# Optimization experiments

Hardware: AMD Instinct MI355X
Metric: run time of the kernel (lower is better)

Reference implementation:

```python
import jax, jax.numpy as jnp
import numpy as np

D_MODEL = 1024
NUM_HEAD = 16
HEAD_DIM = D_MODEL // NUM_HEAD  # 64


def setup_inputs() -> dict:
    key = jax.random.key(0)
    ks = jax.random.split(key, 9)
    B, S = 2, 2048
    s = 0.02
    return {
        "x": jax.random.normal(ks[0], (B, S, D_MODEL), dtype=jnp.float32),
        "Wq": jax.random.normal(ks[1], (D_MODEL, D_MODEL), dtype=jnp.float32) * s,
        "bq": jax.random.normal(ks[2], (D_MODEL,), dtype=jnp.float32) * s,
        "Wk": jax.random.normal(ks[3], (D_MODEL, D_MODEL), dtype=jnp.float32) * s,
        "bk": jax.random.normal(ks[4], (D_MODEL,), dtype=jnp.float32) * s,
        "Wv": jax.random.normal(ks[5], (D_MODEL, D_MODEL), dtype=jnp.float32) * s,
        "bv": jax.random.normal(ks[6], (D_MODEL,), dtype=jnp.float32) * s,
        "Wo": jax.random.normal(ks[7], (D_MODEL, D_MODEL), dtype=jnp.float32) * s,
        "bo": jax.random.normal(ks[8], (D_MODEL,), dtype=jnp.float32) * s,
    }


def _split_head(t):
    # [B,S,D] -> [B,H,S,hd]
    B, S, _ = t.shape
    return t.reshape(B, S, NUM_HEAD, HEAD_DIM).transpose(0, 2, 1, 3)


def reference(x, Wq, bq, Wk, bk, Wv, bv, Wo, bo):
    B, S, D = x.shape
    q = _split_head(x @ Wq.T + bq)  # [B,H,S,hd]
    k = _split_head(x @ Wk.T + bk)
    v = _split_head(x @ Wv.T + bv)
    scale = 1.0 / jnp.sqrt(jnp.asarray(HEAD_DIM, dtype=x.dtype))
    scores = jnp.einsum("bhqd,bhkd->bhqk", q, k) * scale  # [B,H,S,S]
    attn = jax.nn.softmax(scores, axis=-1)
    out = jnp.einsum("bhqk,bhkd->bhqd", attn, v)  # [B,H,S,hd]
    out = out.transpose(0, 2, 1, 3).reshape(B, S, D)
    return out @ Wo.T + bo
```

## Files before the change

### kernel.cpp

```cpp
#include <hip/hip_runtime.h>
#include <cstdint>


typedef unsigned short ush;
typedef __bf16 bf16x8 __attribute__((ext_vector_type(8)));
typedef float f32x4 __attribute__((ext_vector_type(4)));
typedef ush u16x8 __attribute__((ext_vector_type(8)));
typedef ush u16x4 __attribute__((ext_vector_type(4)));
typedef unsigned int u32x4 __attribute__((ext_vector_type(4)));

__device__ __forceinline__ ush f2bf(float f) {
  unsigned int u = __float_as_uint(f);
  u += 0x7fffu + ((u >> 16) & 1u);
  return (ush)(u >> 16);
}

__device__ __forceinline__ unsigned int pack2bf_ru(float a, float b) {
  unsigned int ua = __float_as_uint(a) + 0x8000u;
  unsigned int ub = __float_as_uint(b) + 0x8000u;
  return __builtin_amdgcn_perm(ub, ua, 0x07060302u);
}

__device__ __forceinline__ bf16x8 bc8(u16x8 v) {
  return __builtin_bit_cast(bf16x8, v);
}

__device__ __forceinline__ void async16(const void* g, void* l) {
  __builtin_amdgcn_global_load_lds(
      (const __attribute__((address_space(1))) unsigned int*)(uintptr_t)g,
      (__attribute__((address_space(3))) unsigned int*)(uintptr_t)l, 16, 0, 0);
}

__global__ __launch_bounds__(256) void convert_kernel(
    const float* __restrict__ x, const float* __restrict__ Wq,
    const float* __restrict__ Wk, const float* __restrict__ Wv,
    const float* __restrict__ Wo,
    ush* __restrict__ xb, ush* __restrict__ Wqb, ush* __restrict__ Wkb,
    ush* __restrict__ Wvb, ush* __restrict__ Wob)
{
  int tid = blockIdx.x * 256 + threadIdx.x;
  int base = tid * 4;
  const float* src; ush* dst; int idx;
  if (base < 4194304) { src = x; dst = xb; idx = base; }
  else {
    int r = base - 4194304;
    int seg = r >> 20;
    idx = r & 1048575;
    src = seg == 0 ? Wq : seg == 1 ? Wk : seg == 2 ? Wv : Wo;
    dst = seg == 0 ? Wqb : seg == 1 ? Wkb : seg == 2 ? Wvb : Wob;
  }
  float4 f = *(const float4*)(src + idx);
  u16x4 u = { f2bf(f.x), f2bf(f.y), f2bf(f.z), f2bf(f.w) };
  *(u16x4*)(dst + idx) = u;
}

__device__ __forceinline__ void gemm128_core(
    const ush* __restrict__ gA, const ush* __restrict__ gB,
    int m0, int n0, ush* lA, ush* lB, f32x4 (&acc)[4][4])
{
  const int t = threadIdx.x, w = t >> 6, lane = t & 63;
  const int l15 = lane & 15, quad = lane >> 4;
  const int wm = (w >> 1) * 64, wn = (w & 1) * 64;
#pragma unroll
  for (int i = 0; i < 4; ++i)
#pragma unroll
    for (int j = 0; j < 4; ++j) acc[i][j] = (f32x4){0.f, 0.f, 0.f, 0.f};

  for (int kt = 0; kt < 1024; kt += 64) {
#pragma unroll
    for (int i = 0; i < 4; ++i) {
      int j = i * 256 + w * 64 + lane;
      int row = j >> 3, cc = (j & 7) ^ (row & 7);
      async16(gA + (size_t)(m0 + row) * 1024 + kt + cc * 8,
              lA + (i * 256 + w * 64) * 8);
    }
#pragma unroll
    for (int i = 0; i < 4; ++i) {
      int j = i * 256 + w * 64 + lane;
      int row = j >> 3, cc = (j & 7) ^ (row & 7);
      async16(gB + (size_t)(n0 + row) * 1024 + kt + cc * 8,
              lB + (i * 256 + w * 64) * 8);
    }
    __syncthreads();
#pragma unroll
    for (int kf = 0; kf < 2; ++kf) {
      bf16x8 aF[4], bF[4];
#pragma unroll
      for (int mt = 0; mt < 4; ++mt) {
        int row = wm + mt * 16 + l15;
        aF[mt] = bc8(*(const u16x8*)(lA + row * 64 + (((kf * 4 + quad) ^ (row & 7)) * 8)));
      }
#pragma unroll
      for (int nt = 0; nt < 4; ++nt) {
        int row = wn + nt * 16 + l15;
        bF[nt] = bc8(*(const u16x8*)(lB + row * 64 + (((kf * 4 + quad) ^ (row & 7)) * 8)));
      }
#pragma unroll
      for (int mt = 0; mt < 4; ++mt)
#pragma unroll
        for (int nt = 0; nt < 4; ++nt)
          acc[mt][nt] = __builtin_amdgcn_mfma_f32_16x16x32_bf16(
              aF[mt], bF[nt], acc[mt][nt], 0, 0, 0);
    }
    __syncthreads();
  }
}

__global__ __launch_bounds__(256, 2) void qkv_gemm(
    const ush* __restrict__ xb, const ush* __restrict__ Wqb,
    const ush* __restrict__ Wkb, const ush* __restrict__ Wvb,
    const float* __restrict__ bq, const float* __restrict__ bk,
    const float* __restrict__ bv,
    ush* __restrict__ q, ush* __restrict__ k, ush* __restrict__ vt)
{
  int bid = blockIdx.x;
  int wsel = bid >> 8;
  int rem = bid & 255;
  int m0 = (rem & 31) * 128;
  int n0 = (rem >> 5) * 128;
  const ush* gB = wsel == 0 ? Wqb : wsel == 1 ? Wkb : Wvb;
  const float* bias = wsel == 0 ? bq : wsel == 1 ? bk : bv;
  const float oscale = wsel == 1 ? 0.180336880f : 1.0f;

  __shared__ alignas(16) ush lA[128 * 64];
  __shared__ alignas(16) ush lB[128 * 64];
  f32x4 acc[4][4];
  gemm128_core(xb, gB, m0, n0, lA, lB, acc);

  const int t = threadIdx.x, w = t >> 6, lane = t & 63;
  const int l15 = lane & 15, quad = lane >> 4;
  const int wm = (w >> 1) * 64, wn = (w & 1) * 64;
  if (wsel == 2) {
#pragma unroll
    for (int nt = 0; nt < 4; ++nt) {
      int o = n0 + wn + nt * 16 + l15;
      float bl = bias[o];
      int h = o >> 6, d = o & 63;
#pragma unroll
      for (int mt = 0; mt < 4; ++mt) {
        int tb = m0 + wm + mt * 16 + quad * 4;
        int b = tb >> 11, s = tb & 2047;
        int so = s & 63;
        int sp = (s & ~63) | (so & 35) | ((so & 12) << 1) | ((so & 16) >> 2);
        u16x4 pk = { f2bf(acc[mt][nt][0] + bl), f2bf(acc[mt][nt][1] + bl),
                     f2bf(acc[mt][nt][2] + bl), f2bf(acc[mt][nt][3] + bl) };
        *(u16x4*)(vt + (size_t)(((b * 16 + h) * 64) + d) * 2048 + sp) = pk;
      }
    }
  } else {
    ush* dst = wsel == 0 ? q : k;
#pragma unroll
    for (int nt = 0; nt < 4; ++nt) {
      int o = n0 + wn + nt * 16 + l15;
      float bl = bias[o];
      int h = o >> 6, d = o & 63;
#pragma unroll
      for (int mt = 0; mt < 4; ++mt)
#pragma unroll
        for (int r = 0; r < 4; ++r) {
          int token = m0 + wm + mt * 16 + quad * 4 + r;
          int b = token >> 11, s = token & 2047;
          dst[(size_t)(((b * 16 + h) * 2048) + s) * 64 + d] =
              f2bf((acc[mt][nt][r] + bl) * oscale);
        }
    }
  }
}

__global__ __launch_bounds__(128, 2) void attn_kernel(
    const ush* __restrict__ Q, const ush* __restrict__ K,
    const ush* __restrict__ VT, ush* __restrict__ O)
{
  const int bid = blockIdx.x;
  const int bh = (bid & 7) * 4 + (bid >> 8);
  const int qt = (bid >> 3) & 31;
  const ush* qb = Q + (size_t)bh * 2048 * 64;
  const ush* kb = K + (size_t)bh * 2048 * 64;
  const ush* vtb = VT + (size_t)bh * 64 * 2048;
  const int t = threadIdx.x, w = t >> 6, lane = t & 63;
  const int l15 = lane & 15, quad = lane >> 4;
  const int q0 = qt * 64 + w * 32;

  __shared__ alignas(16) ush lK[2][64 * 64];
  __shared__ alignas(16) ush lV[2][64 * 64];

  const int r0 = t >> 3;
  const int c0 = (t & 7) ^ (r0 & 7);
  const ush* kSrc = kb + (size_t)r0 * 64 + c0 * 8;
  const ush* vSrc = vtb + (size_t)r0 * 2048 + c0 * 8;

  bf16x8 qF[2][2];
#pragma unroll
  for (int g = 0; g < 2; ++g)
#pragma unroll
    for (int kf = 0; kf < 2; ++kf)
      qF[g][kf] = bc8(*(const u16x8*)(qb + (size_t)(q0 + g * 16 + l15) * 64 +
                                      kf * 32 + quad * 8));

  float li[2] = {0.f, 0.f};
  f32x4 accO[2][4];
#pragma unroll
  for (int g = 0; g < 2; ++g)
#pragma unroll
    for (int dt = 0; dt < 4; ++dt) accO[g][dt] = (f32x4){0.f, 0.f, 0.f, 0.f};

#pragma unroll
  for (int i = 0; i < 4; ++i) {
    async16(kSrc + i * 1024, lK[0] + (i * 128 + t) * 8);
    async16(vSrc + (size_t)i * 16 * 2048, lV[0] + (i * 128 + t) * 8);
  }
  __syncthreads();

  for (int it = 0; it < 32; ++it) {
    const int cur = it & 1, nxt = cur ^ 1;
    if (it + 1 < 32) {
      const size_t ko = (size_t)(it + 1) * 64 * 64;
      const int vo = (it + 1) * 64;
#pragma unroll
      for (int i = 0; i < 4; ++i) {
        async16(kSrc + ko + i * 1024, lK[nxt] + (i * 128 + t) * 8);
        async16(vSrc + vo + (size_t)i * 16 * 2048, lV[nxt] + (i * 128 + t) * 8);
      }
    }
    const ush* lk = lK[cur];
    const ush* lv = lV[cur];

    f32x4 sc[2][4];
#pragma unroll
    for (int g = 0; g < 2; ++g)
#pragma unroll
      for (int mt = 0; mt < 4; ++mt) sc[g][mt] = (f32x4){0.f, 0.f, 0.f, 0.f};
#pragma unroll
    for (int kf = 0; kf < 2; ++kf) {
#pragma unroll
      for (int mt = 0; mt < 4; ++mt) {
        int row = mt * 16 + l15;
        bf16x8 aK = bc8(*(const u16x8*)(lk + row * 64 + (((kf * 4 + quad) ^ (row & 7)) * 8)));
#pragma unroll
        for (int g = 0; g < 2; ++g)
          sc[g][mt] = __builtin_amdgcn_mfma_f32_16x16x32_bf16(
              aK, qF[g][kf], sc[g][mt], 0, 0, 0);
      }
    }

    float rs[2] = {0.f, 0.f};
#pragma unroll
    for (int g = 0; g < 2; ++g) {
#pragma unroll
      for (int mt = 0; mt < 4; ++mt)
#pragma unroll
        for (int r = 0; r < 4; ++r) {
          sc[g][mt][r] = __builtin_amdgcn_exp2f(sc[g][mt][r]);
          rs[g] += sc[g][mt][r];
        }
      rs[g] += __shfl_xor(rs[g], 16);
      rs[g] += __shfl_xor(rs[g], 32);
      li[g] += rs[g];
    }

#pragma unroll
    for (int ks = 0; ks < 2; ++ks) {
      bf16x8 aV[4];
#pragma unroll
      for (int dt = 0; dt < 4; ++dt)
        aV[dt] = bc8(*(const u16x8*)(lv + (dt * 16 + l15) * 64 +
                                     (((ks * 4 + quad) ^ (l15 & 7)) * 8)));
#pragma unroll
      for (int g = 0; g < 2; ++g) {
        u32x4 bw = { pack2bf_ru(sc[g][2 * ks][0],     sc[g][2 * ks][1]),
                     pack2bf_ru(sc[g][2 * ks][2],     sc[g][2 * ks][3]),
                     pack2bf_ru(sc[g][2 * ks + 1][0], sc[g][2 * ks + 1][1]),
                     pack2bf_ru(sc[g][2 * ks + 1][2], sc[g][2 * ks + 1][3]) };
        bf16x8 bP = __builtin_bit_cast(bf16x8, bw);
#pragma unroll
        for (int dt = 0; dt < 4; ++dt)
          accO[g][dt] = __builtin_amdgcn_mfma_f32_16x16x32_bf16(
              aV[dt], bP, accO[g][dt], 0, 0, 0);
      }
    }
    __syncthreads();
  }

  const int b = bh >> 4, h = bh & 15;
#pragma unroll
  for (int g = 0; g < 2; ++g) {
    const float linv = __builtin_amdgcn_rcpf(li[g]);
    const int s = q0 + g * 16 + l15;
#pragma unroll
    for (int dt = 0; dt < 4; ++dt) {
      u16x4 pk = { f2bf(accO[g][dt][0] * linv), f2bf(accO[g][dt][1] * linv),
                   f2bf(accO[g][dt][2] * linv), f2bf(accO[g][dt][3] * linv) };
      *(u16x4*)(O + (size_t)(b * 2048 + s) * 1024 + h * 64 + dt * 16 + quad * 4) = pk;
    }
  }
}

__global__ __launch_bounds__(256, 2) void out_gemm(
    const ush* __restrict__ ab, const ush* __restrict__ Wob,
    const float* __restrict__ bo, float* __restrict__ out)
{
  int rem = blockIdx.x;
  int m0 = (rem & 31) * 128;
  int n0 = (rem >> 5) * 128;
  __shared__ alignas(16) ush lA[128 * 64];
  __shared__ alignas(16) ush lB[128 * 64];
  f32x4 acc[4][4];
  gemm128_core(ab, Wob, m0, n0, lA, lB, acc);

  const int t = threadIdx.x, w = t >> 6, lane = t & 63;
  const int l15 = lane & 15, quad = lane >> 4;
  const int wm = (w >> 1) * 64, wn = (w & 1) * 64;
#pragma unroll
  for (int nt = 0; nt < 4; ++nt) {
    int o = n0 + wn + nt * 16 + l15;
    float bl = bo[o];
#pragma unroll
    for (int mt = 0; mt < 4; ++mt)
#pragma unroll
      for (int r = 0; r < 4; ++r) {
        int token = m0 + wm + mt * 16 + quad * 4 + r;
        out[(size_t)token * 1024 + o] = acc[mt][nt][r] + bl;
      }
  }
}

extern "C" void kernel_launch(void* const* d_in, const int* in_sizes, int n_in,
                              void* d_out, int out_size, void* d_ws, size_t ws_size,
                              hipStream_t stream)
{
  const float* x  = (const float*)d_in[0];
  const float* Wq = (const float*)d_in[1];
  const float* bq = (const float*)d_in[2];
  const float* Wk = (const float*)d_in[3];
  const float* bk = (const float*)d_in[4];
  const float* Wv = (const float*)d_in[5];
  const float* bv = (const float*)d_in[6];
  const float* Wo = (const float*)d_in[7];
  const float* bo = (const float*)d_in[8];
  float* out = (float*)d_out;

  char* ws = (char*)d_ws;
  ush* xb  = (ush*)(ws);
  ush* Wqb = (ush*)(ws + (size_t)( 8u << 20));
  ush* Wkb = (ush*)(ws + (size_t)(10u << 20));
  ush* Wvb = (ush*)(ws + (size_t)(12u << 20));
  ush* Wob = (ush*)(ws + (size_t)(14u << 20));
  ush* qb  = (ush*)(ws + (size_t)(16u << 20));
  ush* kb  = (ush*)(ws + (size_t)(24u << 20));
  ush* vtb = (ush*)(ws + (size_t)(32u << 20));
  ush* ab  = (ush*)(ws + (size_t)(40u << 20));

  convert_kernel<<<8192, 256, 0, stream>>>(x, Wq, Wk, Wv, Wo,
                                           xb, Wqb, Wkb, Wvb, Wob);
  qkv_gemm<<<768, 256, 0, stream>>>(xb, Wqb, Wkb, Wvb, bq, bk, bv, qb, kb, vtb);
  attn_kernel<<<1024, 128, 0, stream>>>(qb, kb, vtb, ab);
  out_gemm<<<256, 256, 0, stream>>>(ab, Wob, bo, out);
}
```

Before: 186.9 us.

## Split attention key tile across waves and reduce partial outputs in LDS

Changes the attention work split so each of the two waves processes all 64 queries of the block but only half (32) of the keys in each tile, instead of each wave owning 32 queries over all keys. Each wave loads half the K rows and the matching V columns from LDS, which cuts per-wave LDS fragment reads. Partial outputs and row sums are combined through shared memory after the loop. This doubles the Q fragment and accumulator register footprint per wave and adds an epilogue reduction with an extra barrier, which may hurt occupancy.

```diff
diff --git a/kernel.cpp b/kernel.cpp
--- a/kernel.cpp
+++ b/kernel.cpp
@@ -179,7 +179,7 @@
   const ush* vtb = VT + (size_t)bh * 64 * 2048;
   const int t = threadIdx.x, w = t >> 6, lane = t & 63;
   const int l15 = lane & 15, quad = lane >> 4;
-  const int q0 = qt * 64 + w * 32;
+  const int q0 = qt * 64;
 
   __shared__ alignas(16) ush lK[2][64 * 64];
   __shared__ alignas(16) ush lV[2][64 * 64];
@@ -189,18 +189,18 @@
   const ush* kSrc = kb + (size_t)r0 * 64 + c0 * 8;
   const ush* vSrc = vtb + (size_t)r0 * 2048 + c0 * 8;
 
-  bf16x8 qF[2][2];
-#pragma unroll
-  for (int g = 0; g < 2; ++g)
+  bf16x8 qF[4][2];
+#pragma unroll
+  for (int g = 0; g < 4; ++g)
 #pragma unroll
     for (int kf = 0; kf < 2; ++kf)
       qF[g][kf] = bc8(*(const u16x8*)(qb + (size_t)(q0 + g * 16 + l15) * 64 +
                                       kf * 32 + quad * 8));
 
-  float li[2] = {0.f, 0.f};
-  f32x4 accO[2][4];
-#pragma unroll
-  for (int g = 0; g < 2; ++g)
+  float li[4] = {0.f, 0.f, 0.f, 0.f};
+  f32x4 accO[4][4];
+#pragma unroll
+  for (int g = 0; g < 4; ++g)
 #pragma unroll
     for (int dt = 0; dt < 4; ++dt) accO[g][dt] = (f32x4){0.f, 0.f, 0.f, 0.f};
 
@@ -225,71 +225,85 @@
     const ush* lk = lK[cur];
     const ush* lv = lV[cur];
 
-    f32x4 sc[2][4];
-#pragma unroll
-    for (int g = 0; g < 2; ++g)
-#pragma unroll
-      for (int mt = 0; mt < 4; ++mt) sc[g][mt] = (f32x4){0.f, 0.f, 0.f, 0.f};
+    f32x4 sc[4][2];
+#pragma unroll
+    for (int g = 0; g < 4; ++g)
+#pragma unroll
+      for (int mt = 0; mt < 2; ++mt) sc[g][mt] = (f32x4){0.f, 0.f, 0.f, 0.f};
 #pragma unroll
     for (int kf = 0; kf < 2; ++kf) {
 #pragma unroll
-      for (int mt = 0; mt < 4; ++mt) {
-        int row = mt * 16 + l15;
+      for (int mt = 0; mt < 2; ++mt) {
+        int row = (2 * w + mt) * 16 + l15;
         bf16x8 aK = bc8(*(const u16x8*)(lk + row * 64 + (((kf * 4 + quad) ^ (row & 7)) * 8)));
 #pragma unroll
-        for (int g = 0; g < 2; ++g)
+        for (int g = 0; g < 4; ++g)
           sc[g][mt] = __builtin_amdgcn_mfma_f32_16x16x32_bf16(
               aK, qF[g][kf], sc[g][mt], 0, 0, 0);
       }
     }
 
-    float rs[2] = {0.f, 0.f};
-#pragma unroll
-    for (int g = 0; g < 2; ++g) {
-#pragma unroll
-      for (int mt = 0; mt < 4; ++mt)
+#pragma unroll
+    for (int g = 0; g < 4; ++g) {
+      float rs = 0.f;
+#pragma unroll
+      for (int mt = 0; mt < 2; ++mt)
 #pragma unroll
         for (int r = 0; r < 4; ++r) {
           sc[g][mt][r] = __builtin_amdgcn_exp2f(sc[g][mt][r]);
-          rs[g] += sc[g][mt][r];
+          rs += sc[g][mt][r];
         }
-      rs[g] += __shfl_xor(rs[g], 16);
-      rs[g] += __shfl_xor(rs[g], 32);
-      li[g] += rs[g];
-    }
-
-#pragma unroll
-    for (int ks = 0; ks < 2; ++ks) {
-      bf16x8 aV[4];
+      rs += __shfl_xor(rs, 16);
+      rs += __shfl_xor(rs, 32);
+      li[g] += rs;
+    }
+
+    bf16x8 aV[4];
+#pragma unroll
+    for (int dt = 0; dt < 4; ++dt)
+      aV[dt] = bc8(*(const u16x8*)(lv + (dt * 16 + l15) * 64 +
+                                   (((w * 4 + quad) ^ (l15 & 7)) * 8)));
+#pragma unroll
+    for (int g = 0; g < 4; ++g) {
+      u32x4 bw = { pack2bf_ru(sc[g][0][0], sc[g][0][1]),
+                   pack2bf_ru(sc[g][0][2], sc[g][0][3]),
+                   pack2bf_ru(sc[g][1][0], sc[g][1][1]),
+                   pack2bf_ru(sc[g][1][2], sc[g][1][3]) };
+      bf16x8 bP = __builtin_bit_cast(bf16x8, bw);
 #pragma unroll
       for (int dt = 0; dt < 4; ++dt)
-        aV[dt] = bc8(*(const u16x8*)(lv + (dt * 16 + l15) * 64 +
-                                     (((ks * 4 + quad) ^ (l15 & 7)) * 8)));
-#pragma unroll
-      for (int g = 0; g < 2; ++g) {
-        u32x4 bw = { pack2bf_ru(sc[g][2 * ks][0],     sc[g][2 * ks][1]),
-                     pack2bf_ru(sc[g][2 * ks][2],     sc[g][2 * ks][3]),
-                     pack2bf_ru(sc[g][2 * ks + 1][0], sc[g][2 * ks + 1][1]),
-                     pack2bf_ru(sc[g][2 * ks + 1][2], sc[g][2 * ks + 1][3]) };
-        bf16x8 bP = __builtin_bit_cast(bf16x8, bw);
-#pragma unroll
-        for (int dt = 0; dt < 4; ++dt)
-          accO[g][dt] = __builtin_amdgcn_mfma_f32_16x16x32_bf16(
-              aV[dt], bP, accO[g][dt], 0, 0, 0);
-      }
+        accO[g][dt] = __builtin_amdgcn_mfma_f32_16x16x32_bf16(
+            aV[dt], bP, accO[g][dt], 0, 0, 0);
     }
     __syncthreads();
   }
 
+  float* redO = (float*)lK;
+  float* redL = (float*)lV;
+  const int ow = 1 - w;
+#pragma unroll
+  for (int j = 0; j < 2; ++j) {
+    int fg = ow * 2 + j;
+#pragma unroll
+    for (int dt = 0; dt < 4; ++dt)
+      *(f32x4*)(redO + (((w * 2 + j) * 4 + dt) * 64 + lane) * 4) = accO[fg][dt];
+    redL[(w * 2 + j) * 64 + lane] = li[fg];
+  }
+  __syncthreads();
   const int b = bh >> 4, h = bh & 15;
 #pragma unroll
-  for (int g = 0; g < 2; ++g) {
-    const float linv = __builtin_amdgcn_rcpf(li[g]);
-    const int s = q0 + g * 16 + l15;
+  for (int j = 0; j < 2; ++j) {
+    int mg = w * 2 + j;
+#pragma unroll
+    for (int dt = 0; dt < 4; ++dt)
+      accO[mg][dt] += *(const f32x4*)(redO + (((ow * 2 + j) * 4 + dt) * 64 + lane) * 4);
+    float lsum = li[mg] + redL[(ow * 2 + j) * 64 + lane];
+    const float linv = __builtin_amdgcn_rcpf(lsum);
+    const int s = q0 + mg * 16 + l15;
 #pragma unroll
     for (int dt = 0; dt < 4; ++dt) {
-      u16x4 pk = { f2bf(accO[g][dt][0] * linv), f2bf(accO[g][dt][1] * linv),
-                   f2bf(accO[g][dt][2] * linv), f2bf(accO[g][dt][3] * linv) };
+      u16x4 pk = { f2bf(accO[mg][dt][0] * linv), f2bf(accO[mg][dt][1] * linv),
+                   f2bf(accO[mg][dt][2] * linv), f2bf(accO[mg][dt][3] * linv) };
       *(u16x4*)(O + (size_t)(b * 2048 + s) * 1024 + h * 64 + dt * 16 + quad * 4) = pk;
     }
   }
```

Result: slower. 408.4 us (+118.5%).
